# Performance work log

Measured on AMD Instinct MI355X. Metric: run time of the kernel, lower is better.

Reference implementation:

```python
import jax, jax.numpy as jnp
import numpy as np

H = 128   # hidden_size
B = 8
TQ = 512  # num queries
TK = 512  # num keys


def setup_inputs() -> dict:
    key = jax.random.key(0)
    ks = jax.random.split(key, 8)
    s = 1.0 / np.sqrt(H)  # torch Linear default init bound
    return {
        "queries": jax.random.normal(ks[0], (B, TQ, H), dtype=jnp.float32),
        "keys": jax.random.normal(ks[1], (B, TK, H), dtype=jnp.float32),
        "Wa_w": jax.random.uniform(ks[2], (H, H), jnp.float32, -s, s),
        "Wa_b": jax.random.uniform(ks[3], (H,), jnp.float32, -s, s),
        "Ua_w": jax.random.uniform(ks[4], (H, H), jnp.float32, -s, s),
        "Ua_b": jax.random.uniform(ks[5], (H,), jnp.float32, -s, s),
        "Va_w": jax.random.uniform(ks[6], (H,), jnp.float32, -s, s),
        "Va_b": jax.random.uniform(ks[7], (), jnp.float32, -s, s),
    }


def reference(queries, keys, Wa_w, Wa_b, Ua_w, Ua_b, Va_w, Va_b):
    # Linear projections (torch Linear: y = x @ W.T + b)
    q = queries @ Wa_w.T + Wa_b                  # (B, Tq, H)
    k = keys @ Ua_w.T + Ua_b                     # (B, Tk, H)
    # Additive (Bahdanau) scores with broadcast intermediate (B, Tq, Tk, H)
    e = jnp.tanh(q[:, :, None, :] + k[:, None, :, :])
    scores = jnp.einsum('bqkh,h->bqk', e, Va_w) + Va_b  # (B, Tq, Tk)
    weights = jax.nn.softmax(scores, axis=-1)            # softmax over keys
    contexts = jnp.einsum('bqk,bkh->bqh', weights, keys) # (B, Tq, H)
    return contexts, weights
```

## Files before the change

### kernel.cpp

```cpp
#include <hip/hip_runtime.h>
#include <hip/hip_bf16.h>
#include <stdint.h>

#define HD 128
#define NB 8
#define TQN 512
#define TKN 512
#define QT 8
#define KTILE 64
#define KSTR 132
#define QSTR 132
#define KBSTR 136
#define FQT 8

typedef __attribute__((ext_vector_type(8))) short short8;
typedef __attribute__((ext_vector_type(4))) float f32x4;
typedef __attribute__((ext_vector_type(2))) float f32x2;

#if __has_builtin(__builtin_elementwise_fma)
#define FMA2(a,b,c) __builtin_elementwise_fma((a),(b),(c))
#else
#define FMA2(a,b,c) ((a)*(b)+(c))
#endif

static __device__ __forceinline__ float lo16(uint32_t w){
  union { uint32_t i; float f; } v; v.i = w << 16; return v.f;
}
static __device__ __forceinline__ float hi16(uint32_t w){
  union { uint32_t i; float f; } v; v.i = w & 0xffff0000u; return v.f;
}
static __device__ __forceinline__ float bf2f(unsigned short u){
  union { uint32_t i; float f; } v; v.i = ((uint32_t)u) << 16; return v.f;
}
static __device__ __forceinline__ uint32_t f2bf(float f){
  union { float f; uint32_t i; } v; v.f = f;
  uint32_t u = v.i;
  u += 0x7fffu + ((u >> 16) & 1u);
  return u >> 16;
}
static __device__ __forceinline__ float tanh_acc(float x){
  float e = __builtin_amdgcn_exp2f(x * 2.8853900817779268f);
  return fmaf(-2.0f, __builtin_amdgcn_rcpf(e + 1.0f), 1.0f);
}
template<int CTRL>
static __device__ __forceinline__ float dpp_add(float x){
  union { float f; int i; } u; u.f = x;
  int y = __builtin_amdgcn_update_dpp(0, u.i, CTRL, 0xf, 0xf, true);
  union { int i; float f; } w; w.i = y;
  return x + w.f;
}
static __device__ __forceinline__ float ld1(const void* p, size_t idx, bool f32){
  return f32 ? ((const float*)p)[idx] : bf2f(((const unsigned short*)p)[idx]);
}
static __device__ __forceinline__ short8 ld8bf(const void* p, size_t idx, bool f32){
  short8 r;
  if (f32){
    const float* s = (const float*)p + idx;
    #pragma unroll
    for (int i = 0; i < 8; i++) r[i] = (short)f2bf(s[i]);
  } else {
    r = *(const short8*)((const unsigned short*)p + idx);
  }
  return r;
}

__global__ __launch_bounds__(256) void proj_kernel(
    const void* __restrict__ queries, const void* __restrict__ keys,
    const void* __restrict__ Wa_w,   const void* __restrict__ Wa_b,
    const void* __restrict__ Ua_w,   const void* __restrict__ Ua_b,
    float* __restrict__ tq_g, unsigned short* __restrict__ tk_gb)
{
  __shared__ unsigned int flg_s[8];
  const int tid = threadIdx.x;
  if (tid < 8) flg_s[tid] = 0;
  __syncthreads();
  {
    const void* ptrs[6] = {queries, keys, Wa_w, Wa_b, Ua_w, Ua_b};
    const int grp = tid >> 5;
    const int l   = tid & 31;
    if (grp < 6){
      const unsigned short* p = (const unsigned short*)ptrs[grp];
      unsigned short a = p[2*l], c = p[64 + 2*l];
      if (((a >> 7) & 0xFF) > 0x90 || ((c >> 7) & 0xFF) > 0x90)
        atomicOr(&flg_s[grp], 1u);
    }
  }
  __syncthreads();
  const int lane = tid & 63, wv = tid >> 6, ln = lane & 15, quad = lane >> 4;
  const int b7  = blockIdx.x & 7;
  const int idx = blockIdx.x >> 3;
  const int row0 = (idx < 32) ? (b7*TQN + idx*16)
                              : (NB*TQN + b7*TKN + (idx-32)*16);

  const void* x; const void* W; const void* bias; int r;
  bool fx, fw, fb;
  const bool isK = (row0 >= NB*TQN);
  if (!isK){
    x = queries; W = Wa_w; bias = Wa_b; r = row0;
    fx = flg_s[0] != 0; fw = flg_s[2] != 0; fb = flg_s[3] != 0;
  } else {
    x = keys; W = Ua_w; bias = Ua_b; r = row0 - NB*TQN;
    fx = flg_s[1] != 0; fw = flg_s[4] != 0; fb = flg_s[5] != 0;
  }

  short8 a[4];
  #pragma unroll
  for (int ks = 0; ks < 4; ks++)
    a[ks] = ld8bf(x, (size_t)(r + ln)*HD + ks*32 + quad*8, fx);

  #pragma unroll
  for (int nt = 0; nt < 2; nt++){
    const int h0 = (2*wv + nt)*16;
    f32x4 c = {0.f,0.f,0.f,0.f};
    #pragma unroll
    for (int ks = 0; ks < 4; ks++)
      c = __builtin_amdgcn_mfma_f32_16x16x32_bf16(
            a[ks], ld8bf(W, (size_t)(h0 + ln)*HD + ks*32 + quad*8, fw), c, 0,0,0);
    const float wb = ld1(bias, h0 + ln, fb);
    #pragma unroll
    for (int r4 = 0; r4 < 4; r4++){
      const float e = __builtin_amdgcn_exp2f((c[r4] + wb) * 2.8853900817779268f);
      const float ec = fminf(fmaxf(e, 0x1p-13f), 0x1p13f);
      const size_t di = (size_t)(r + quad*4 + r4)*HD + h0 + ln;
      if (isK) tk_gb[di] = (unsigned short)f2bf(ec);
      else     tq_g[di]  = ec;
    }
  }
}

__global__ __launch_bounds__(1024, 8) void attn_kernel(
    const void* __restrict__ queries, const void* __restrict__ keys,
    const void* __restrict__ Va_w,
    const float* __restrict__ tq_g, const unsigned short* __restrict__ tk_gb,
    void* __restrict__ out)
{
  __shared__ __align__(16) unsigned short tkb_s[2][KTILE*KBSTR];
  __shared__ float wgt_s[QT*TKN];
  __shared__ unsigned int flg_s[4];

  const int tid = threadIdx.x;
  const int b     = blockIdx.x & 7;
  const int qbase = (blockIdx.x >> 3) * QT;

  uint4 st;
  {
    const uint4* src = (const uint4*)(tk_gb + (size_t)(b*TKN)*HD);
    st = src[tid];
  }

  if (tid < 4) flg_s[tid] = 0;
  __syncthreads();
  {
    const void* ptrs[3] = {queries, keys, Va_w};
    const int grp = tid >> 5;
    const int l   = tid & 31;
    if (grp < 3){
      const unsigned short* p = (const unsigned short*)ptrs[grp];
      unsigned short a = p[2*l], c = p[64 + 2*l];
      if (((a >> 7) & 0xFF) > 0x90 || ((c >> 7) & 0xFF) > 0x90)
        atomicOr(&flg_s[grp], 1u);
    }
  }
  __syncthreads();
  const bool fQ  = flg_s[0] != 0;
  const bool fK  = flg_s[1] != 0;
  const bool fVw = flg_s[2] != 0;

  const int lane = tid & 63;
  const int wv   = tid >> 6;
  const int qr   = wv & 7;
  const int hh   = wv >> 3;
  const int ln   = lane & 15;
  const int quad = lane >> 4;
  const int s8   = lane >> 3;
  const int o8   = lane & 7;
  const int sk   = tid >> 4;
  const int shh  = (tid & 15) * 8;

  f32x2 eq2[4], a2[4];
  {
    const float* qsrc = tq_g + (size_t)(b*TQN + qbase + qr)*HD + o8*16 + hh*8;
    #pragma unroll
    for (int c = 0; c < 2; c++){
      const float4 t = *(const float4*)(qsrc + c*4);
      eq2[2*c].x = t.x; eq2[2*c].y = t.y;
      eq2[2*c+1].x = t.z; eq2[2*c+1].y = t.w;
      a2[2*c].x   = -2.0f * ld1(Va_w, o8*16 + hh*8 + c*4 + 0, fVw);
      a2[2*c].y   = -2.0f * ld1(Va_w, o8*16 + hh*8 + c*4 + 1, fVw);
      a2[2*c+1].x = -2.0f * ld1(Va_w, o8*16 + hh*8 + c*4 + 2, fVw);
      a2[2*c+1].y = -2.0f * ld1(Va_w, o8*16 + hh*8 + c*4 + 3, fVw);
    }
  }
  f32x2 one2; one2.x = 1.f; one2.y = 1.f;

  *(uint4*)(&tkb_s[0][sk*KBSTR + shh]) = st;
  __syncthreads();

  float sc8[8];
  for (int kt = 0; kt < 8; kt++){
    if (kt < 7){
      const uint4* src = (const uint4*)(tk_gb + (size_t)(b*TKN + (kt+1)*KTILE)*HD);
      st = src[tid];
    }
    const unsigned short* buf = &tkb_s[kt & 1][0];

    float acc[8];
    #pragma unroll
    for (int i = 0; i < 8; i++){
      const unsigned short* tk = buf + (i*8 + s8)*KBSTR + o8*16 + hh*8;
      const uint4 v = *(const uint4*)tk;
      float acci = 0.f;
      {
        f32x2 kv0; kv0.x = lo16(v.x); kv0.y = hi16(v.x);
        f32x2 kv1; kv1.x = lo16(v.y); kv1.y = hi16(v.y);
        f32x2 x01 = FMA2(eq2[0], kv0, one2);
        f32x2 x23 = FMA2(eq2[1], kv1, one2);
        f32x2 xs01; xs01.x = x01.y; xs01.y = x01.x;
        f32x2 xs23; xs23.x = x23.y; xs23.y = x23.x;
        f32x2 s01 = a2[0] * xs01;
        f32x2 s23 = a2[1] * xs23;
        const float p01 = x01.x * x01.y;
        const float p23 = x23.x * x23.y;
        const float n01 = s01.x + s01.y;
        const float n23 = s23.x + s23.y;
        const float P   = p01 * p23;
        const float N   = fmaf(n01, p23, n23 * p01);
        acci = fmaf(N, __builtin_amdgcn_rcpf(P), acci);
      }
      {
        f32x2 kv0; kv0.x = lo16(v.z); kv0.y = hi16(v.z);
        f32x2 kv1; kv1.x = lo16(v.w); kv1.y = hi16(v.w);
        f32x2 x01 = FMA2(eq2[2], kv0, one2);
        f32x2 x23 = FMA2(eq2[3], kv1, one2);
        f32x2 xs01; xs01.x = x01.y; xs01.y = x01.x;
        f32x2 xs23; xs23.x = x23.y; xs23.y = x23.x;
        f32x2 s01 = a2[2] * xs01;
        f32x2 s23 = a2[3] * xs23;
        const float p01 = x01.x * x01.y;
        const float p23 = x23.x * x23.y;
        const float n01 = s01.x + s01.y;
        const float n23 = s23.x + s23.y;
        const float P   = p01 * p23;
        const float N   = fmaf(n01, p23, n23 * p01);
        acci = fmaf(N, __builtin_amdgcn_rcpf(P), acci);
      }
      acc[i] = acci;
    }
    #pragma unroll
    for (int i = 0; i < 8; i++){
      float a = acc[i];
      a = dpp_add<0xB1>(a);
      a = dpp_add<0x4E>(a);
      a = dpp_add<0x141>(a);
      acc[i] = a;
    }
    float sc = acc[0];
    #pragma unroll
    for (int i = 1; i < 8; i++) sc = (o8 == i) ? acc[i] : sc;
    sc8[kt] = sc;

    if (kt < 7)
      *(uint4*)(&tkb_s[(kt+1) & 1][sk*KBSTR + shh]) = st;
    __syncthreads();
  }

  float* psc = (float*)&tkb_s[0][0];
  if (hh == 1){
    #pragma unroll
    for (int kt = 0; kt < 8; kt++)
      psc[qr*TKN + kt*64 + o8*8 + s8] = sc8[kt];
  }
  __syncthreads();
  if (hh == 0){
    float vals[8];
    float m = -1e30f;
    #pragma unroll
    for (int j = 0; j < 8; j++){
      vals[j] = sc8[j] + psc[qr*TKN + j*64 + o8*8 + s8];
      m = fmaxf(m, vals[j]);
    }
    #pragma unroll
    for (int o = 32; o > 0; o >>= 1) m = fmaxf(m, __shfl_xor(m, o));
    float sum = 0.f;
    #pragma unroll
    for (int j = 0; j < 8; j++){
      vals[j] = __builtin_amdgcn_exp2f((vals[j]-m)*1.4426950408889634f);
      sum += vals[j];
    }
    #pragma unroll
    for (int o = 32; o > 0; o >>= 1) sum += __shfl_xor(sum, o);
    const float inv = __builtin_amdgcn_rcpf(sum);
    const int psrc = ((((lane & 7) << 3) | (lane >> 3)) << 2);
    const size_t wbase = (size_t)NB*TQN*HD + (size_t)(b*TQN + qbase + qr)*TKN;
    float* wrow = wgt_s + qr*TKN;
    #pragma unroll
    for (int j = 0; j < 8; j++){
      union { float f; int i; } u; u.f = vals[j]*inv;
      union { int i; float f; } t; t.i = __builtin_amdgcn_ds_bpermute(psrc, u.i);
      wrow[j*64 + lane] = t.f;
      if (fQ) ((float*)out)[wbase + j*64 + lane] = t.f;
      else    ((unsigned short*)out)[wbase + j*64 + lane] = (unsigned short)f2bf(t.f);
    }
  }
  __syncthreads();

  {
    const int p2 = wv & 3;
    const int g2 = wv >> 2;
    const int h0 = ln * 8;
    f32x2 a0v[4], a1v[4];
    #pragma unroll
    for (int t = 0; t < 4; t++){
      a0v[t].x = 0.f; a0v[t].y = 0.f;
      a1v[t].x = 0.f; a1v[t].y = 0.f;
    }
    const float* w0rb = wgt_s + (2*p2)*TKN;
    if (!fK){
      const unsigned short* kb = (const unsigned short*)keys
          + (size_t)(b*TKN)*HD + h0;
      #pragma unroll
      for (int t = 0; t < 2; t++){
        const int kt = g2*2 + t;
        const float* w0r = w0rb + kt*KTILE;
        const float* w1r = w0r + TKN;
        #pragma unroll
        for (int i = 0; i < 16; i++){
          const int k = i*4 + quad;
          const uint4 v = *(const uint4*)(kb + (size_t)(kt*KTILE + k)*HD);
          const float w0 = w0r[k];
          const float w1 = w1r[k];
          f32x2 c0; c0.x = lo16(v.x); c0.y = hi16(v.x);
          f32x2 c1; c1.x = lo16(v.y); c1.y = hi16(v.y);
          f32x2 c2; c2.x = lo16(v.z); c2.y = hi16(v.z);
          f32x2 c3; c3.x = lo16(v.w); c3.y = hi16(v.w);
          f32x2 w0v; w0v.x = w0; w0v.y = w0;
          f32x2 w1v; w1v.x = w1; w1v.y = w1;
          a0v[0] = FMA2(w0v, c0, a0v[0]); a0v[1] = FMA2(w0v, c1, a0v[1]);
          a0v[2] = FMA2(w0v, c2, a0v[2]); a0v[3] = FMA2(w0v, c3, a0v[3]);
          a1v[0] = FMA2(w1v, c0, a1v[0]); a1v[1] = FMA2(w1v, c1, a1v[1]);
          a1v[2] = FMA2(w1v, c2, a1v[2]); a1v[3] = FMA2(w1v, c3, a1v[3]);
        }
      }
    } else {
      const float* kb = (const float*)keys + (size_t)(b*TKN)*HD + h0;
      #pragma unroll
      for (int t = 0; t < 2; t++){
        const int kt = g2*2 + t;
        const float* w0r = w0rb + kt*KTILE;
        const float* w1r = w0r + TKN;
        #pragma unroll
        for (int i = 0; i < 16; i++){
          const int k = i*4 + quad;
          const float* kr = kb + (size_t)(kt*KTILE + k)*HD;
          const float4 k0 = *(const float4*)(kr);
          const float4 k1 = *(const float4*)(kr + 4);
          const float w0 = w0r[k];
          const float w1 = w1r[k];
          f32x2 c0; c0.x = k0.x; c0.y = k0.y;
          f32x2 c1; c1.x = k0.z; c1.y = k0.w;
          f32x2 c2; c2.x = k1.x; c2.y = k1.y;
          f32x2 c3; c3.x = k1.z; c3.y = k1.w;
          f32x2 w0v; w0v.x = w0; w0v.y = w0;
          f32x2 w1v; w1v.x = w1; w1v.y = w1;
          a0v[0] = FMA2(w0v, c0, a0v[0]); a0v[1] = FMA2(w0v, c1, a0v[1]);
          a0v[2] = FMA2(w0v, c2, a0v[2]); a0v[3] = FMA2(w0v, c3, a0v[3]);
          a1v[0] = FMA2(w1v, c0, a1v[0]); a1v[1] = FMA2(w1v, c1, a1v[1]);
          a1v[2] = FMA2(w1v, c2, a1v[2]); a1v[3] = FMA2(w1v, c3, a1v[3]);
        }
      }
    }
    float a0[8], a1[8];
    #pragma unroll
    for (int t = 0; t < 4; t++){
      a0[2*t] = a0v[t].x; a0[2*t+1] = a0v[t].y;
      a1[2*t] = a1v[t].x; a1[2*t+1] = a1v[t].y;
    }
    #pragma unroll
    for (int t = 0; t < 8; t++){
      a0[t] += __shfl_xor(a0[t], 16); a0[t] += __shfl_xor(a0[t], 32);
      a1[t] += __shfl_xor(a1[t], 16); a1[t] += __shfl_xor(a1[t], 32);
    }
    __syncthreads();
    float* part = psc;
    if (g2 > 0 && quad == 0){
      const int base = ((g2-1)*8 + 2*p2)*HD + h0;
      *(float4*)(part + base       ) = (float4){a0[0],a0[1],a0[2],a0[3]};
      *(float4*)(part + base + 4   ) = (float4){a0[4],a0[5],a0[6],a0[7]};
      *(float4*)(part + base + HD  ) = (float4){a1[0],a1[1],a1[2],a1[3]};
      *(float4*)(part + base + HD+4) = (float4){a1[4],a1[5],a1[6],a1[7]};
    }
    __syncthreads();
    if (g2 == 0 && quad == 0){
      #pragma unroll
      for (int gg = 0; gg < 3; gg++){
        const int base = (gg*8 + 2*p2)*HD + h0;
        const float4 q00 = *(const float4*)(part + base);
        const float4 q01 = *(const float4*)(part + base + 4);
        const float4 q10 = *(const float4*)(part + base + HD);
        const float4 q11 = *(const float4*)(part + base + HD + 4);
        a0[0]+=q00.x; a0[1]+=q00.y; a0[2]+=q00.z; a0[3]+=q00.w;
        a0[4]+=q01.x; a0[5]+=q01.y; a0[6]+=q01.z; a0[7]+=q01.w;
        a1[0]+=q10.x; a1[1]+=q10.y; a1[2]+=q10.z; a1[3]+=q10.w;
        a1[4]+=q11.x; a1[5]+=q11.y; a1[6]+=q11.z; a1[7]+=q11.w;
      }
      const size_t crow0 = (size_t)(b*TQN + qbase + 2*p2    )*HD + h0;
      const size_t crow1 = (size_t)(b*TQN + qbase + 2*p2 + 1)*HD + h0;
      if (fQ){
        float* oc = (float*)out;
        *(float4*)(oc + crow0)     = (float4){a0[0],a0[1],a0[2],a0[3]};
        *(float4*)(oc + crow0 + 4) = (float4){a0[4],a0[5],a0[6],a0[7]};
        *(float4*)(oc + crow1)     = (float4){a1[0],a1[1],a1[2],a1[3]};
        *(float4*)(oc + crow1 + 4) = (float4){a1[4],a1[5],a1[6],a1[7]};
      } else {
        uint4 o0, o1;
        o0.x = f2bf(a0[0]) | (f2bf(a0[1]) << 16);
        o0.y = f2bf(a0[2]) | (f2bf(a0[3]) << 16);
        o0.z = f2bf(a0[4]) | (f2bf(a0[5]) << 16);
        o0.w = f2bf(a0[6]) | (f2bf(a0[7]) << 16);
        o1.x = f2bf(a1[0]) | (f2bf(a1[1]) << 16);
        o1.y = f2bf(a1[2]) | (f2bf(a1[3]) << 16);
        o1.z = f2bf(a1[4]) | (f2bf(a1[5]) << 16);
        o1.w = f2bf(a1[6]) | (f2bf(a1[7]) << 16);
        *(uint4*)((unsigned short*)out + crow0) = o0;
        *(uint4*)((unsigned short*)out + crow1) = o1;
      }
    }
  }
}

__global__ __launch_bounds__(512, 4) void fused_kernel(
    const void* __restrict__ queries, const void* __restrict__ keys,
    const void* __restrict__ Wa_w,   const void* __restrict__ Wa_b,
    const void* __restrict__ Ua_w,   const void* __restrict__ Ua_b,
    const void* __restrict__ Va_w,
    void* __restrict__ out)
{
  __shared__ float qp_s[FQT*QSTR];
  __shared__ float va_s[HD];
  __shared__ __align__(16) unsigned short keys_s[KTILE*KBSTR];
  __shared__ __align__(16) float kp_s[KTILE*KSTR];
  __shared__ float sc_s[FQT*TKN];
  __shared__ unsigned int flg_s[8];

  const int tid = threadIdx.x;
  if (tid < 8) flg_s[tid] = 0;
  __syncthreads();
  {
    const void* ptrs[7] = {queries, keys, Wa_w, Wa_b, Ua_w, Ua_b, Va_w};
    const int grp = tid >> 5;
    const int l   = tid & 31;
    if (grp < 7){
      const unsigned short* p = (const unsigned short*)ptrs[grp];
      unsigned short a = p[2*l], c = p[64 + 2*l];
      if (((a >> 7) & 0xFF) > 0x90 || ((c >> 7) & 0xFF) > 0x90)
        atomicOr(&flg_s[grp], 1u);
    }
  }
  __syncthreads();
  const bool fQ  = flg_s[0] != 0;
  const bool fK  = flg_s[1] != 0;
  const bool fWw = flg_s[2] != 0;
  const bool fWb = flg_s[3] != 0;
  const bool fUw = flg_s[4] != 0;
  const bool fUb = flg_s[5] != 0;
  const bool fVw = flg_s[6] != 0;

  const int lane = tid & 63;
  const int wv   = tid >> 6;
  const int ln   = lane & 15;
  const int quad = lane >> 4;
  const int b     = blockIdx.x >> 6;
  const int qbase = (blockIdx.x & 63) * FQT;

  if (tid < HD) va_s[tid] = ld1(Va_w, tid, fVw);
  {
    const int h0 = wv * 16;
    const size_t qrow = (size_t)(b*TQN + qbase + (ln & 7))*HD;
    f32x4 c = {0.f,0.f,0.f,0.f};
    #pragma unroll
    for (int ks = 0; ks < 4; ks++){
      short8 a = ld8bf(queries, qrow + ks*32 + quad*8, fQ);
      short8 w = ld8bf(Wa_w, (size_t)(h0 + ln)*HD + ks*32 + quad*8, fWw);
      c = __builtin_amdgcn_mfma_f32_16x16x32_bf16(a, w, c, 0,0,0);
    }
    const float wb = ld1(Wa_b, h0 + ln, fWb);
    #pragma unroll
    for (int r = 0; r < 4; r++){
      const int row = quad*4 + r;
      if (row < FQT) qp_s[row*QSTR + h0 + ln] = tanh_acc(c[r] + wb);
    }
  }
  short8 ub[4];
  float ubias;
  {
    const int h0 = wv * 16;
    #pragma unroll
    for (int ks = 0; ks < 4; ks++)
      ub[ks] = ld8bf(Ua_w, (size_t)(h0 + ln)*HD + ks*32 + quad*8, fUw);
    ubias = ld1(Ua_b, h0 + ln, fUb);
  }
  {
    if (fK){
      const float4* src = (const float4*)((const float*)keys + (size_t)(b*TKN)*HD);
      #pragma unroll
      for (int j = 0; j < 4; j++){
        const int f = tid + 512*j;
        float4 v = src[f];
        const int k = f >> 5, h = (f & 31)*4;
        uint2 p;
        p.x = f2bf(v.x) | (f2bf(v.y) << 16);
        p.y = f2bf(v.z) | (f2bf(v.w) << 16);
        *(uint2*)(keys_s + k*KBSTR + h) = p;
      }
    } else {
      const uint4* src = (const uint4*)((const unsigned short*)keys + (size_t)(b*TKN)*HD);
      #pragma unroll
      for (int j = 0; j < 2; j++){
        const int f = tid + 512*j;
        uint4 v = src[f];
        const int k = f >> 4, h = (f & 15)*8;
        *(uint4*)(keys_s + k*KBSTR + h) = v;
      }
    }
  }
  __syncthreads();

  const int s8 = lane >> 3;
  const int o8 = lane & 7;
  float tqr[16], var[16], vat[16];
  {
    const float* qsrc = qp_s + wv*QSTR + o8*16;
    const float* vsrc = va_s + o8*16;
    #pragma unroll
    for (int c = 0; c < 4; c++){
      float4 t = *(const float4*)(qsrc + c*4);
      float4 v = *(const float4*)(vsrc + c*4);
      tqr[c*4+0]=t.x; tqr[c*4+1]=t.y; tqr[c*4+2]=t.z; tqr[c*4+3]=t.w;
      var[c*4+0]=v.x; var[c*4+1]=v.y; var[c*4+2]=v.z; var[c*4+3]=v.w;
      vat[c*4+0]=v.x*t.x; vat[c*4+1]=v.y*t.y; vat[c*4+2]=v.z*t.z; vat[c*4+3]=v.w*t.w;
    }
  }
  for (int kt = 0; kt < 8; kt++){
    f32x4 kc[4];
    #pragma unroll
    for (int mt = 0; mt < 4; mt++) kc[mt] = (f32x4){0.f,0.f,0.f,0.f};
    #pragma unroll
    for (int ks = 0; ks < 4; ks++){
      short8 af[4];
      #pragma unroll
      for (int mt = 0; mt < 4; mt++)
        af[mt] = *(const short8*)(keys_s + (mt*16 + ln)*KBSTR + ks*32 + quad*8);
      #pragma unroll
      for (int mt = 0; mt < 4; mt++)
        kc[mt] = __builtin_amdgcn_mfma_f32_16x16x32_bf16(af[mt], ub[ks], kc[mt], 0,0,0);
    }
    __syncthreads();
    #pragma unroll
    for (int mt = 0; mt < 4; mt++)
      #pragma unroll
      for (int r = 0; r < 4; r++)
        kp_s[(mt*16 + quad*4 + r)*KSTR + wv*16 + ln] = tanh_acc(kc[mt][r] + ubias);
    if (kt < 7){
      if (fK){
        const float4* src = (const float4*)((const float*)keys + (size_t)(b*TKN + (kt+1)*KTILE)*HD);
        #pragma unroll
        for (int j = 0; j < 4; j++){
          const int f = tid + 512*j;
          float4 v = src[f];
          const int k = f >> 5, h = (f & 31)*4;
          uint2 p;
          p.x = f2bf(v.x) | (f2bf(v.y) << 16);
          p.y = f2bf(v.z) | (f2bf(v.w) << 16);
          *(uint2*)(keys_s + k*KBSTR + h) = p;
        }
      } else {
        const uint4* src = (const uint4*)((const unsigned short*)keys + (size_t)(b*TKN + (kt+1)*KTILE)*HD);
        #pragma unroll
        for (int j = 0; j < 2; j++){
          const int f = tid + 512*j;
          uint4 v = src[f];
          const int k = f >> 4, h = (f & 15)*8;
          *(uint4*)(keys_s + k*KBSTR + h) = v;
        }
      }
    }
    __syncthreads();
    float acc[8];
    #pragma unroll
    for (int i = 0; i < 8; i++) acc[i] = 0.f;
    #pragma unroll
    for (int i = 0; i < 8; i++){
      const float* tk = kp_s + (i*8 + s8)*KSTR + o8*16;
      #pragma unroll
      for (int c = 0; c < 4; c++){
        const float4 kv = *(const float4*)(tk + c*4);
        acc[i] = fmaf(fmaf(var[c*4+0], kv.x, vat[c*4+0]),
                      __builtin_amdgcn_rcpf(fmaf(tqr[c*4+0], kv.x, 1.f)), acc[i]);
        acc[i] = fmaf(fmaf(var[c*4+1], kv.y, vat[c*4+1]),
                      __builtin_amdgcn_rcpf(fmaf(tqr[c*4+1], kv.y, 1.f)), acc[i]);
        acc[i] = fmaf(fmaf(var[c*4+2], kv.z, vat[c*4+2]),
                      __builtin_amdgcn_rcpf(fmaf(tqr[c*4+2], kv.z, 1.f)), acc[i]);
        acc[i] = fmaf(fmaf(var[c*4+3], kv.w, vat[c*4+3]),
                      __builtin_amdgcn_rcpf(fmaf(tqr[c*4+3], kv.w, 1.f)), acc[i]);
      }
    }
    #pragma unroll
    for (int i = 0; i < 8; i++){
      float a = acc[i];
      a = dpp_add<0xB1>(a);
      a = dpp_add<0x4E>(a);
      a = dpp_add<0x141>(a);
      acc[i] = a;
    }
    float sc = acc[0];
    #pragma unroll
    for (int i = 1; i < 8; i++) sc = (o8 == i) ? acc[i] : sc;
    sc_s[wv*TKN + kt*KTILE + o8*8 + s8] = sc;
  }
  __syncthreads();
  {
    float vals[8];
    float m = -1e30f;
    #pragma unroll
    for (int j = 0; j < 8; j++){
      vals[j] = sc_s[wv*TKN + lane + 64*j];
      m = fmaxf(m, vals[j]);
    }
    #pragma unroll
    for (int o = 32; o > 0; o >>= 1) m = fmaxf(m, __shfl_xor(m, o));
    float sum = 0.f;
    #pragma unroll
    for (int j = 0; j < 8; j++){
      vals[j] = __builtin_amdgcn_exp2f((vals[j]-m)*1.4426950408889634f);
      sum += vals[j];
    }
    #pragma unroll
    for (int o = 32; o > 0; o >>= 1) sum += __shfl_xor(sum, o);
    const float inv = __builtin_amdgcn_rcpf(sum);
    const size_t wbase = (size_t)NB*TQN*HD + (size_t)(b*TQN + qbase + wv)*TKN;
    #pragma unroll
    for (int j = 0; j < 8; j++){
      const float w = vals[j]*inv;
      sc_s[wv*TKN + lane + 64*j] = w;
      if (fQ) ((float*)out)[wbase + lane + 64*j] = w;
      else    ((unsigned short*)out)[wbase + lane + 64*j] = (unsigned short)f2bf(w);
    }
  }
  __syncthreads();
  {
    const int p2 = wv & 3;
    const int g2 = wv >> 2;
    const int h0 = ln * 8;
    float a0[8], a1[8];
    #pragma unroll
    for (int t = 0; t < 8; t++){ a0[t] = 0.f; a1[t] = 0.f; }
    for (int kt = 0; kt < 8; kt++){
      if (fK){
        const float4* src = (const float4*)((const float*)keys + (size_t)(b*TKN + kt*KTILE)*HD);
        #pragma unroll
        for (int j = 0; j < 4; j++){
          const int f = tid + 512*j;
          const int k = f >> 5, h = (f & 31)*4;
          *(float4*)(kp_s + k*KSTR + h) = src[f];
        }
      } else {
        const uint4* src = (const uint4*)((const unsigned short*)keys + (size_t)(b*TKN + kt*KTILE)*HD);
        #pragma unroll
        for (int j = 0; j < 2; j++){
          const int f = tid + 512*j;
          const int k = f >> 4, h = (f & 15)*8;
          uint4 v = src[f];
          float4 d0, d1;
          d0.x = lo16(v.x); d0.y = hi16(v.x); d0.z = lo16(v.y); d0.w = hi16(v.y);
          d1.x = lo16(v.z); d1.y = hi16(v.z); d1.z = lo16(v.w); d1.w = hi16(v.w);
          *(float4*)(kp_s + k*KSTR + h)     = d0;
          *(float4*)(kp_s + k*KSTR + h + 4) = d1;
        }
      }
      __syncthreads();
      const float* w0r = sc_s + (2*p2)*TKN + kt*KTILE + g2*32;
      const float* w1r = w0r + TKN;
      #pragma unroll
      for (int i = 0; i < 8; i++){
        const int k = i*4 + quad;
        const float w0 = w0r[k];
        const float w1 = w1r[k];
        const float* kr = kp_s + (g2*32 + k)*KSTR + h0;
        const float4 k0 = *(const float4*)(kr);
        const float4 k1 = *(const float4*)(kr + 4);
        a0[0]=fmaf(w0,k0.x,a0[0]); a0[1]=fmaf(w0,k0.y,a0[1]);
        a0[2]=fmaf(w0,k0.z,a0[2]); a0[3]=fmaf(w0,k0.w,a0[3]);
        a0[4]=fmaf(w0,k1.x,a0[4]); a0[5]=fmaf(w0,k1.y,a0[5]);
        a0[6]=fmaf(w0,k1.z,a0[6]); a0[7]=fmaf(w0,k1.w,a0[7]);
        a1[0]=fmaf(w1,k0.x,a1[0]); a1[1]=fmaf(w1,k0.y,a1[1]);
        a1[2]=fmaf(w1,k0.z,a1[2]); a1[3]=fmaf(w1,k0.w,a1[3]);
        a1[4]=fmaf(w1,k1.x,a1[4]); a1[5]=fmaf(w1,k1.y,a1[5]);
        a1[6]=fmaf(w1,k1.z,a1[6]); a1[7]=fmaf(w1,k1.w,a1[7]);
      }
      __syncthreads();
    }
    #pragma unroll
    for (int t = 0; t < 8; t++){
      a0[t] += __shfl_xor(a0[t], 16); a0[t] += __shfl_xor(a0[t], 32);
      a1[t] += __shfl_xor(a1[t], 16); a1[t] += __shfl_xor(a1[t], 32);
    }
    float* part = qp_s;
    if (g2 == 1 && quad == 0){
      *(float4*)(part + (2*p2  )*HD + h0    ) = (float4){a0[0],a0[1],a0[2],a0[3]};
      *(float4*)(part + (2*p2  )*HD + h0 + 4) = (float4){a0[4],a0[5],a0[6],a0[7]};
      *(float4*)(part + (2*p2+1)*HD + h0    ) = (float4){a1[0],a1[1],a1[2],a1[3]};
      *(float4*)(part + (2*p2+1)*HD + h0 + 4) = (float4){a1[4],a1[5],a1[6],a1[7]};
    }
    __syncthreads();
    if (g2 == 0 && quad == 0){
      const float4 p00 = *(const float4*)(part + (2*p2  )*HD + h0    );
      const float4 p01 = *(const float4*)(part + (2*p2  )*HD + h0 + 4);
      const float4 p10 = *(const float4*)(part + (2*p2+1)*HD + h0    );
      const float4 p11 = *(const float4*)(part + (2*p2+1)*HD + h0 + 4);
      const size_t crow0 = (size_t)(b*TQN + qbase + 2*p2    )*HD + h0;
      const size_t crow1 = (size_t)(b*TQN + qbase + 2*p2 + 1)*HD + h0;
      if (fQ){
        float* oc = (float*)out;
        *(float4*)(oc + crow0)     = (float4){a0[0]+p00.x, a0[1]+p00.y, a0[2]+p00.z, a0[3]+p00.w};
        *(float4*)(oc + crow0 + 4) = (float4){a0[4]+p01.x, a0[5]+p01.y, a0[6]+p01.z, a0[7]+p01.w};
        *(float4*)(oc + crow1)     = (float4){a1[0]+p10.x, a1[1]+p10.y, a1[2]+p10.z, a1[3]+p10.w};
        *(float4*)(oc + crow1 + 4) = (float4){a1[4]+p11.x, a1[5]+p11.y, a1[6]+p11.z, a1[7]+p11.w};
      } else {
        uint4 o0, o1;
        o0.x = f2bf(a0[0]+p00.x) | (f2bf(a0[1]+p00.y) << 16);
        o0.y = f2bf(a0[2]+p00.z) | (f2bf(a0[3]+p00.w) << 16);
        o0.z = f2bf(a0[4]+p01.x) | (f2bf(a0[5]+p01.y) << 16);
        o0.w = f2bf(a0[6]+p01.z) | (f2bf(a0[7]+p01.w) << 16);
        o1.x = f2bf(a1[0]+p10.x) | (f2bf(a1[1]+p10.y) << 16);
        o1.y = f2bf(a1[2]+p10.z) | (f2bf(a1[3]+p10.w) << 16);
        o1.z = f2bf(a1[4]+p11.x) | (f2bf(a1[5]+p11.y) << 16);
        o1.w = f2bf(a1[6]+p11.z) | (f2bf(a1[7]+p11.w) << 16);
        *(uint4*)((unsigned short*)out + crow0) = o0;
        *(uint4*)((unsigned short*)out + crow1) = o1;
      }
    }
  }
}

extern "C" void kernel_launch(void* const* d_in, const int* in_sizes, int n_in,
                              void* d_out, int out_size, void* d_ws, size_t ws_size,
                              hipStream_t stream) {
  (void)in_sizes; (void)n_in; (void)out_size;
  const size_t need = (size_t)2 * NB * TQN * HD * sizeof(float);
  if (ws_size >= need){
    float* tq_g = (float*)d_ws;
    unsigned short* tk_gb = (unsigned short*)(tq_g + (size_t)NB*TQN*HD);
    proj_kernel<<<512, 256, 0, stream>>>(d_in[0], d_in[1], d_in[2], d_in[3],
                                         d_in[4], d_in[5], tq_g, tk_gb);
    attn_kernel<<<512, 1024, 0, stream>>>(d_in[0], d_in[1], d_in[6],
                                          tq_g, tk_gb, d_out);
  } else {
    fused_kernel<<<512, 512, 0, stream>>>(d_in[0], d_in[1], d_in[2], d_in[3],
                                          d_in[4], d_in[5], d_in[6], d_out);
  }
}
```

Before: 138.3 us.

## Fuse query projection into attention kernel; keep only key projection separate

The query projection (Wa) moves out of the separate projection kernel and into the attention kernel. Each block computes its 8 query rows with an MFMA and stores the tanh-transformed values in shared memory, so the fp32 query workspace write and read-back disappear. The projection kernel now handles keys only, with half as many blocks. The cost is extra MFMA work and Wa_w loads in every attention block, plus a larger shared-memory footprint; the 16-row MFMA also wastes half its rows on 8 queries.

```diff
diff --git a/kernel.cpp b/kernel.cpp
--- a/kernel.cpp
+++ b/kernel.cpp
@@ -64,94 +64,17 @@
   return r;
 }
 
-__global__ __launch_bounds__(256) void proj_kernel(
-    const void* __restrict__ queries, const void* __restrict__ keys,
-    const void* __restrict__ Wa_w,   const void* __restrict__ Wa_b,
-    const void* __restrict__ Ua_w,   const void* __restrict__ Ua_b,
-    float* __restrict__ tq_g, unsigned short* __restrict__ tk_gb)
+__global__ __launch_bounds__(256) void kproj_kernel(
+    const void* __restrict__ keys,
+    const void* __restrict__ Ua_w, const void* __restrict__ Ua_b,
+    unsigned short* __restrict__ tk_gb)
 {
-  __shared__ unsigned int flg_s[8];
+  __shared__ unsigned int flg_s[4];
   const int tid = threadIdx.x;
-  if (tid < 8) flg_s[tid] = 0;
-  __syncthreads();
-  {
-    const void* ptrs[6] = {queries, keys, Wa_w, Wa_b, Ua_w, Ua_b};
-    const int grp = tid >> 5;
-    const int l   = tid & 31;
-    if (grp < 6){
-      const unsigned short* p = (const unsigned short*)ptrs[grp];
-      unsigned short a = p[2*l], c = p[64 + 2*l];
-      if (((a >> 7) & 0xFF) > 0x90 || ((c >> 7) & 0xFF) > 0x90)
-        atomicOr(&flg_s[grp], 1u);
-    }
-  }
-  __syncthreads();
-  const int lane = tid & 63, wv = tid >> 6, ln = lane & 15, quad = lane >> 4;
-  const int b7  = blockIdx.x & 7;
-  const int idx = blockIdx.x >> 3;
-  const int row0 = (idx < 32) ? (b7*TQN + idx*16)
-                              : (NB*TQN + b7*TKN + (idx-32)*16);
-
-  const void* x; const void* W; const void* bias; int r;
-  bool fx, fw, fb;
-  const bool isK = (row0 >= NB*TQN);
-  if (!isK){
-    x = queries; W = Wa_w; bias = Wa_b; r = row0;
-    fx = flg_s[0] != 0; fw = flg_s[2] != 0; fb = flg_s[3] != 0;
-  } else {
-    x = keys; W = Ua_w; bias = Ua_b; r = row0 - NB*TQN;
-    fx = flg_s[1] != 0; fw = flg_s[4] != 0; fb = flg_s[5] != 0;
-  }
-
-  short8 a[4];
-  #pragma unroll
-  for (int ks = 0; ks < 4; ks++)
-    a[ks] = ld8bf(x, (size_t)(r + ln)*HD + ks*32 + quad*8, fx);
-
-  #pragma unroll
-  for (int nt = 0; nt < 2; nt++){
-    const int h0 = (2*wv + nt)*16;
-    f32x4 c = {0.f,0.f,0.f,0.f};
-    #pragma unroll
-    for (int ks = 0; ks < 4; ks++)
-      c = __builtin_amdgcn_mfma_f32_16x16x32_bf16(
-            a[ks], ld8bf(W, (size_t)(h0 + ln)*HD + ks*32 + quad*8, fw), c, 0,0,0);
-    const float wb = ld1(bias, h0 + ln, fb);
-    #pragma unroll
-    for (int r4 = 0; r4 < 4; r4++){
-      const float e = __builtin_amdgcn_exp2f((c[r4] + wb) * 2.8853900817779268f);
-      const float ec = fminf(fmaxf(e, 0x1p-13f), 0x1p13f);
-      const size_t di = (size_t)(r + quad*4 + r4)*HD + h0 + ln;
-      if (isK) tk_gb[di] = (unsigned short)f2bf(ec);
-      else     tq_g[di]  = ec;
-    }
-  }
-}
-
-__global__ __launch_bounds__(1024, 8) void attn_kernel(
-    const void* __restrict__ queries, const void* __restrict__ keys,
-    const void* __restrict__ Va_w,
-    const float* __restrict__ tq_g, const unsigned short* __restrict__ tk_gb,
-    void* __restrict__ out)
-{
-  __shared__ __align__(16) unsigned short tkb_s[2][KTILE*KBSTR];
-  __shared__ float wgt_s[QT*TKN];
-  __shared__ unsigned int flg_s[4];
-
-  const int tid = threadIdx.x;
-  const int b     = blockIdx.x & 7;
-  const int qbase = (blockIdx.x >> 3) * QT;
-
-  uint4 st;
-  {
-    const uint4* src = (const uint4*)(tk_gb + (size_t)(b*TKN)*HD);
-    st = src[tid];
-  }
-
   if (tid < 4) flg_s[tid] = 0;
   __syncthreads();
   {
-    const void* ptrs[3] = {queries, keys, Va_w};
+    const void* ptrs[3] = {keys, Ua_w, Ua_b};
     const int grp = tid >> 5;
     const int l   = tid & 31;
     if (grp < 3){
@@ -162,9 +85,79 @@
     }
   }
   __syncthreads();
+  const bool fK  = flg_s[0] != 0;
+  const bool fUw = flg_s[1] != 0;
+  const bool fUb = flg_s[2] != 0;
+
+  const int lane = tid & 63, wv = tid >> 6, ln = lane & 15, quad = lane >> 4;
+  const int b7  = blockIdx.x & 7;
+  const int idx = blockIdx.x >> 3;
+  const int r   = b7*TKN + idx*16;
+
+  short8 a[4];
+  #pragma unroll
+  for (int ks = 0; ks < 4; ks++)
+    a[ks] = ld8bf(keys, (size_t)(r + ln)*HD + ks*32 + quad*8, fK);
+
+  #pragma unroll
+  for (int nt = 0; nt < 2; nt++){
+    const int h0 = (2*wv + nt)*16;
+    f32x4 c = {0.f,0.f,0.f,0.f};
+    #pragma unroll
+    for (int ks = 0; ks < 4; ks++)
+      c = __builtin_amdgcn_mfma_f32_16x16x32_bf16(
+            a[ks], ld8bf(Ua_w, (size_t)(h0 + ln)*HD + ks*32 + quad*8, fUw), c, 0,0,0);
+    const float wb = ld1(Ua_b, h0 + ln, fUb);
+    #pragma unroll
+    for (int r4 = 0; r4 < 4; r4++){
+      const float e = __builtin_amdgcn_exp2f((c[r4] + wb) * 2.8853900817779268f);
+      tk_gb[(size_t)(r + quad*4 + r4)*HD + h0 + ln] =
+          (unsigned short)f2bf(fminf(fmaxf(e, 0x1p-13f), 0x1p13f));
+    }
+  }
+}
+
+__global__ __launch_bounds__(1024, 8) void attn_kernel(
+    const void* __restrict__ queries, const void* __restrict__ keys,
+    const void* __restrict__ Wa_w,   const void* __restrict__ Wa_b,
+    const void* __restrict__ Va_w,
+    const unsigned short* __restrict__ tk_gb,
+    void* __restrict__ out)
+{
+  __shared__ __align__(16) unsigned short tkb_s[2][KTILE*KBSTR];
+  __shared__ float wgt_s[QT*TKN];
+  __shared__ float qp_s[QT*QSTR];
+  __shared__ unsigned int flg_s[8];
+
+  const int tid = threadIdx.x;
+  const int b     = blockIdx.x & 7;
+  const int qbase = (blockIdx.x >> 3) * QT;
+
+  uint4 st;
+  {
+    const uint4* src = (const uint4*)(tk_gb + (size_t)(b*TKN)*HD);
+    st = src[tid];
+  }
+
+  if (tid < 8) flg_s[tid] = 0;
+  __syncthreads();
+  {
+    const void* ptrs[5] = {queries, keys, Wa_w, Wa_b, Va_w};
+    const int grp = tid >> 5;
+    const int l   = tid & 31;
+    if (grp < 5){
+      const unsigned short* p = (const unsigned short*)ptrs[grp];
+      unsigned short a = p[2*l], c = p[64 + 2*l];
+      if (((a >> 7) & 0xFF) > 0x90 || ((c >> 7) & 0xFF) > 0x90)
+        atomicOr(&flg_s[grp], 1u);
+    }
+  }
+  __syncthreads();
   const bool fQ  = flg_s[0] != 0;
   const bool fK  = flg_s[1] != 0;
-  const bool fVw = flg_s[2] != 0;
+  const bool fWw = flg_s[2] != 0;
+  const bool fWb = flg_s[3] != 0;
+  const bool fVw = flg_s[4] != 0;
 
   const int lane = tid & 63;
   const int wv   = tid >> 6;
@@ -177,9 +170,33 @@
   const int sk   = tid >> 4;
   const int shh  = (tid & 15) * 8;
 
+  if (wv < 8){
+    const int h0 = wv * 16;
+    const size_t qrow = (size_t)(b*TQN + qbase + (ln & 7))*HD;
+    f32x4 c = {0.f,0.f,0.f,0.f};
+    #pragma unroll
+    for (int ks = 0; ks < 4; ks++){
+      short8 a = ld8bf(queries, qrow + ks*32 + quad*8, fQ);
+      short8 w = ld8bf(Wa_w, (size_t)(h0 + ln)*HD + ks*32 + quad*8, fWw);
+      c = __builtin_amdgcn_mfma_f32_16x16x32_bf16(a, w, c, 0,0,0);
+    }
+    const float wb = ld1(Wa_b, h0 + ln, fWb);
+    #pragma unroll
+    for (int r4 = 0; r4 < 4; r4++){
+      const int row = quad*4 + r4;
+      if (row < QT){
+        const float e = __builtin_amdgcn_exp2f((c[r4] + wb) * 2.8853900817779268f);
+        qp_s[row*QSTR + h0 + ln] = fminf(fmaxf(e, 0x1p-13f), 0x1p13f);
+      }
+    }
+  }
+
+  *(uint4*)(&tkb_s[0][sk*KBSTR + shh]) = st;
+  __syncthreads();
+
   f32x2 eq2[4], a2[4];
   {
-    const float* qsrc = tq_g + (size_t)(b*TQN + qbase + qr)*HD + o8*16 + hh*8;
+    const float* qsrc = qp_s + qr*QSTR + o8*16 + hh*8;
     #pragma unroll
     for (int c = 0; c < 2; c++){
       const float4 t = *(const float4*)(qsrc + c*4);
@@ -192,9 +209,6 @@
     }
   }
   f32x2 one2; one2.x = 1.f; one2.y = 1.f;
-
-  *(uint4*)(&tkb_s[0][sk*KBSTR + shh]) = st;
-  __syncthreads();
 
   float sc8[8];
   for (int kt = 0; kt < 8; kt++){
@@ -746,14 +760,12 @@
                               void* d_out, int out_size, void* d_ws, size_t ws_size,
                               hipStream_t stream) {
   (void)in_sizes; (void)n_in; (void)out_size;
-  const size_t need = (size_t)2 * NB * TQN * HD * sizeof(float);
+  const size_t need = (size_t)NB * TKN * HD * sizeof(unsigned short) * 2;
   if (ws_size >= need){
-    float* tq_g = (float*)d_ws;
-    unsigned short* tk_gb = (unsigned short*)(tq_g + (size_t)NB*TQN*HD);
-    proj_kernel<<<512, 256, 0, stream>>>(d_in[0], d_in[1], d_in[2], d_in[3],
-                                         d_in[4], d_in[5], tq_g, tk_gb);
-    attn_kernel<<<512, 1024, 0, stream>>>(d_in[0], d_in[1], d_in[6],
-                                          tq_g, tk_gb, d_out);
+    unsigned short* tk_gb = (unsigned short*)d_ws;
+    kproj_kernel<<<256, 256, 0, stream>>>(d_in[1], d_in[4], d_in[5], tk_gb);
+    attn_kernel<<<512, 1024, 0, stream>>>(d_in[0], d_in[1], d_in[2], d_in[3],
+                                          d_in[6], tk_gb, d_out);
   } else {
     fused_kernel<<<512, 512, 0, stream>>>(d_in[0], d_in[1], d_in[2], d_in[3],
                                           d_in[4], d_in[5], d_in[6], d_out);
```

New measurement: 143.7 us. +3.9%, slower.
